# Performance work log

Measured on AMD Instinct MI355X. Metric: run time of the kernel, lower is better.

The kernel has to match this reference:

```python
import jax, jax.numpy as jnp
import numpy as np

B, L, HP, H, W = 4, 32, 32, 64, 64
D, DFFN, MAXL = 32, 64, 128

def setup_inputs() -> dict:
    key = jax.random.key(0)
    ks = jax.random.split(key, 20)
    rn = lambda k, s, sc=0.1: jax.random.normal(k, s, jnp.float32) * sc
    return {
        'x': jax.random.normal(ks[0], (B, 2 * L * HP, H, W), jnp.float32),
        'in_proj_w': rn(ks[1], (D, 12)), 'in_proj_b': rn(ks[2], (D,)),
        'layer_emb': rn(ks[3], (MAXL, D)),
        'time_decay': rn(ks[4], (D,)), 'time_first': rn(ks[5], (D,)),
        'ln_tm_g': jnp.ones((D,)), 'ln_tm_b': jnp.zeros((D,)),
        'tm_r': rn(ks[6], (D, D)), 'tm_k': rn(ks[7], (D, D)),
        'tm_v': rn(ks[8], (D, D)), 'tm_out': rn(ks[9], (D, D)),
        'ln_cm_g': jnp.ones((D,)), 'ln_cm_b': jnp.zeros((D,)),
        'cm_k': rn(ks[10], (DFFN, D)), 'cm_v': rn(ks[11], (D, DFFN)), 'cm_r': rn(ks[12], (D, D)),
        'gate_w': rn(ks[13], (1, D)), 'gate_b': rn(ks[14], (1,)),
        'row_w': rn(ks[15], (H, D)), 'row_b': rn(ks[16], (H,)),
        'col_w': rn(ks[17], (W, D)), 'col_b': rn(ks[18], (W,)),
    }

def _ln(x, g, b, eps=1e-5):
    mu = x.mean(-1, keepdims=True)
    var = ((x - mu) ** 2).mean(-1, keepdims=True)
    return (x - mu) * jax.lax.rsqrt(var + eps) * g + b

def _stats(a, b):
    # a, b: [B, L, HP, H, W] -> [B, L, HP, 12]
    af = a.reshape(*a.shape[:-2], -1)
    bf = b.reshape(*b.shape[:-2], -1)
    hs = lambda f: jnp.stack([f.mean(-1), f.std(-1, ddof=1), f.min(-1), f.max(-1)], -1)
    d = af - bf
    dm = d.mean(-1, keepdims=True)
    ds = d.std(-1, ddof=1, keepdims=True)
    dl2 = jnp.linalg.norm(d, axis=-1, keepdims=True)
    na = jnp.maximum(jnp.linalg.norm(af, axis=-1), 1e-8)
    nb = jnp.maximum(jnp.linalg.norm(bf, axis=-1), 1e-8)
    cos = ((af * bf).sum(-1) / (na * nb))[..., None]
    return jnp.concatenate([hs(af), hs(bf), dm, ds, dl2, cos], -1)

def reference(x, in_proj_w, in_proj_b, layer_emb, time_decay, time_first,
              ln_tm_g, ln_tm_b, tm_r, tm_k, tm_v, tm_out,
              ln_cm_g, ln_cm_b, cm_k, cm_v, cm_r,
              gate_w, gate_b, row_w, row_b, col_w, col_b):
    n = L * HP
    a = x[:, :n].reshape(B, L, HP, H, W)
    b = x[:, n:].reshape(B, L, HP, H, W)
    stats = _stats(a, b)                                   # [B,L,HP,12]
    feat_in = jnp.einsum('blhs,ds->blhd', stats, in_proj_w) + in_proj_b \
        + layer_emb[:L][None, :, None, :]
    feat_in = jnp.transpose(feat_in, (1, 0, 2, 3))         # [L,B,HP,D]
    wdec = jnp.exp(time_decay)

    def step(state, f):
        aa, bb, pp = state
        xn = _ln(f, ln_tm_g, ln_tm_b)
        r = jax.nn.sigmoid(xn @ tm_r.T)
        k = xn @ tm_k.T
        v = xn @ tm_v.T
        ww = time_first + k
        p = jnp.maximum(pp, ww)
        e1 = jnp.exp(pp - p)
        e2 = jnp.exp(ww - p)
        wkv = (e1 * aa + e2 * v) / jnp.maximum(e1 * bb + e2, 1e-8)
        ww2 = pp - wdec
        p2 = jnp.maximum(ww2, k)
        e1b = jnp.exp(ww2 - p2)
        e2b = jnp.exp(k - p2)
        y = f + r * (wkv @ tm_out.T)
        xn2 = _ln(y, ln_cm_g, ln_cm_b)
        kk = jnp.square(jax.nn.relu(xn2 @ cm_k.T))
        y = y + jax.nn.sigmoid(xn2 @ cm_r.T) * (kk @ cm_v.T)
        return (e1b * aa + e2b * v, e1b * bb + e2b, p2), y

    z = jnp.zeros((B, HP, D), x.dtype)
    init = (z, z, jnp.full((B, HP, D), -1e30, x.dtype))
    _, feats = jax.lax.scan(step, init, feat_in)           # [L,B,HP,D]

    gate = feats @ gate_w.T + gate_b                       # [L,B,HP,1]
    row = feats @ row_w.T + row_b                          # [L,B,HP,H]
    col = feats @ col_w.T + col_b                          # [L,B,HP,W]
    mask = jax.nn.sigmoid(gate[..., None] + row[..., None] + col[..., None, :])
    aT = jnp.transpose(a, (1, 0, 2, 3, 4))
    bT = jnp.transpose(b, (1, 0, 2, 3, 4))
    merged = mask * aT + (1.0 - mask) * bT                 # [L,B,HP,H,W]
    mixed = jnp.transpose(merged, (1, 0, 2, 3, 4)).reshape(B, n, H, W)
    return mixed, jax.nn.sigmoid(gate).mean(), mask.mean()
```

## Files before the change

### kernel.cpp

```cpp
#include <hip/hip_runtime.h>
#include <math.h>


__device__ __forceinline__ float sigf(float v) { return 1.0f / (1.0f + __expf(-v)); }

__device__ __forceinline__ float bl(float v, int l) {
    return __int_as_float(__builtin_amdgcn_readlane(__float_as_int(v), l));
}

__global__ __launch_bounds__(256) void k_stats(
    const float* __restrict__ x, const float* __restrict__ in_proj_w,
    const float* __restrict__ in_proj_b, const float* __restrict__ layer_emb,
    float* __restrict__ feat)
{
    __shared__ float red[4][9];
    __shared__ float tot[9];
    const int bid = blockIdx.x;
    const int hp = bid & 31, l = (bid >> 5) & 31, bb = bid >> 10;
    const float4* pa = (const float4*)(x + (size_t)(bb * 2048 + l * 32 + hp) * 4096);
    const float4* pb = (const float4*)(x + (size_t)(bb * 2048 + 1024 + l * 32 + hp) * 4096);
    const int t = threadIdx.x;

    float sa = 0.f, saa = 0.f, sb = 0.f, sbb = 0.f, sab = 0.f;
    float mna = 3.4e38f, mxa = -3.4e38f, mnb = 3.4e38f, mxb = -3.4e38f;
#pragma unroll
    for (int it = 0; it < 4; ++it) {
        float4 a4 = pa[t + it * 256];
        float4 b4 = pb[t + it * 256];
        sa  += a4.x + a4.y + a4.z + a4.w;
        sb  += b4.x + b4.y + b4.z + b4.w;
        saa += a4.x * a4.x + a4.y * a4.y + a4.z * a4.z + a4.w * a4.w;
        sbb += b4.x * b4.x + b4.y * b4.y + b4.z * b4.z + b4.w * b4.w;
        sab += a4.x * b4.x + a4.y * b4.y + a4.z * b4.z + a4.w * b4.w;
        mna = fminf(mna, fminf(fminf(a4.x, a4.y), fminf(a4.z, a4.w)));
        mxa = fmaxf(mxa, fmaxf(fmaxf(a4.x, a4.y), fmaxf(a4.z, a4.w)));
        mnb = fminf(mnb, fminf(fminf(b4.x, b4.y), fminf(b4.z, b4.w)));
        mxb = fmaxf(mxb, fmaxf(fmaxf(b4.x, b4.y), fmaxf(b4.z, b4.w)));
    }
#pragma unroll
    for (int m = 1; m < 64; m <<= 1) {
        sa  += __shfl_xor(sa, m);
        saa += __shfl_xor(saa, m);
        sb  += __shfl_xor(sb, m);
        sbb += __shfl_xor(sbb, m);
        sab += __shfl_xor(sab, m);
        mna = fminf(mna, __shfl_xor(mna, m));
        mxa = fmaxf(mxa, __shfl_xor(mxa, m));
        mnb = fminf(mnb, __shfl_xor(mnb, m));
        mxb = fmaxf(mxb, __shfl_xor(mxb, m));
    }
    const int lane = t & 63, wv = t >> 6;
    if (lane == 0) {
        red[wv][0] = sa;  red[wv][1] = saa; red[wv][2] = sb;  red[wv][3] = sbb;
        red[wv][4] = sab; red[wv][5] = mna; red[wv][6] = mxa; red[wv][7] = mnb;
        red[wv][8] = mxb;
    }
    __syncthreads();
    if (t == 0) {
#pragma unroll
        for (int q = 0; q < 5; ++q) tot[q] = red[0][q] + red[1][q] + red[2][q] + red[3][q];
        tot[5] = fminf(fminf(red[0][5], red[1][5]), fminf(red[2][5], red[3][5]));
        tot[6] = fmaxf(fmaxf(red[0][6], red[1][6]), fmaxf(red[2][6], red[3][6]));
        tot[7] = fminf(fminf(red[0][7], red[1][7]), fminf(red[2][7], red[3][7]));
        tot[8] = fmaxf(fmaxf(red[0][8], red[1][8]), fmaxf(red[2][8], red[3][8]));
    }
    __syncthreads();
    if (t < 32) {
        const float SA = tot[0], SAA = tot[1], SB = tot[2], SBB = tot[3], SAB = tot[4];
        const float inv_n = 1.f / 4096.f, inv_nm1 = 1.f / 4095.f;
        float st[12];
        st[0] = SA * inv_n;
        st[1] = sqrtf(fmaxf(SAA - SA * SA * inv_n, 0.f) * inv_nm1);
        st[2] = tot[5]; st[3] = tot[6];
        st[4] = SB * inv_n;
        st[5] = sqrtf(fmaxf(SBB - SB * SB * inv_n, 0.f) * inv_nm1);
        st[6] = tot[7]; st[7] = tot[8];
        const float SD = SA - SB, SDD = SAA - 2.f * SAB + SBB;
        st[8]  = SD * inv_n;
        st[9]  = sqrtf(fmaxf(SDD - SD * SD * inv_n, 0.f) * inv_nm1);
        st[10] = sqrtf(fmaxf(SDD, 0.f));
        const float na = fmaxf(sqrtf(SAA), 1e-8f), nb2 = fmaxf(sqrtf(SBB), 1e-8f);
        st[11] = SAB / (na * nb2);
        float acc = in_proj_b[t] + layer_emb[l * 32 + t];
#pragma unroll
        for (int s2 = 0; s2 < 12; ++s2) acc += st[s2] * in_proj_w[t * 12 + s2];
        feat[((l * 4 + bb) * 32 + hp) * 32 + t] = acc;
    }
}

__global__ __launch_bounds__(64, 1) void k_scan(
    const float* __restrict__ feat,
    const float* __restrict__ time_decay, const float* __restrict__ time_first,
    const float* __restrict__ ln_tm_g, const float* __restrict__ ln_tm_b,
    const float* __restrict__ tm_r, const float* __restrict__ tm_k,
    const float* __restrict__ tm_v, const float* __restrict__ tm_out,
    const float* __restrict__ ln_cm_g, const float* __restrict__ ln_cm_b,
    const float* __restrict__ cm_k, const float* __restrict__ cm_v,
    const float* __restrict__ cm_r, float* __restrict__ feats_out)
{
    const int t = threadIdx.x;
    const int d = t & 31;

    float w_r[32], w_k[32], w_v[32], w_o[32], w_cr[32], w_ck[32], w_cv[64];
    {
        const float4* pr = (const float4*)(tm_r  + d * 32);
        const float4* pk = (const float4*)(tm_k  + d * 32);
        const float4* pv = (const float4*)(tm_v  + d * 32);
        const float4* po = (const float4*)(tm_out + d * 32);
        const float4* pc = (const float4*)(cm_r  + d * 32);
        const float4* pq = (const float4*)(cm_k  + t * 32);
        const float4* pw = (const float4*)(cm_v  + d * 64);
#pragma unroll
        for (int jq = 0; jq < 8; ++jq) {
            float4 v;
            v = pr[jq]; w_r[4*jq] = v.x; w_r[4*jq+1] = v.y; w_r[4*jq+2] = v.z; w_r[4*jq+3] = v.w;
            v = pk[jq]; w_k[4*jq] = v.x; w_k[4*jq+1] = v.y; w_k[4*jq+2] = v.z; w_k[4*jq+3] = v.w;
            v = pv[jq]; w_v[4*jq] = v.x; w_v[4*jq+1] = v.y; w_v[4*jq+2] = v.z; w_v[4*jq+3] = v.w;
            v = po[jq]; w_o[4*jq] = v.x; w_o[4*jq+1] = v.y; w_o[4*jq+2] = v.z; w_o[4*jq+3] = v.w;
            v = pc[jq]; w_cr[4*jq] = v.x; w_cr[4*jq+1] = v.y; w_cr[4*jq+2] = v.z; w_cr[4*jq+3] = v.w;
            v = pq[jq]; w_ck[4*jq] = v.x; w_ck[4*jq+1] = v.y; w_ck[4*jq+2] = v.z; w_ck[4*jq+3] = v.w;
        }
#pragma unroll
        for (int jq = 0; jq < 16; ++jq) {
            float4 v = pw[jq];
            w_cv[4*jq] = v.x; w_cv[4*jq+1] = v.y; w_cv[4*jq+2] = v.z; w_cv[4*jq+3] = v.w;
        }
    }
    const float gt = ln_tm_g[d], bt = ln_tm_b[d];
    const float gc = ln_cm_g[d], bc = ln_cm_b[d];
    const float tf = time_first[d];
    const float wd = __expf(time_decay[d]);
    const int seq = blockIdx.x;
    const int bb = seq >> 5, hp = seq & 31;
    const int base = (bb * 32 + hp) * 32 + d;

    float aa = 0.f, bbs = 0.f, pp = -1e30f;
    float f = feat[base];

    for (int l = 0; l < 32; ++l) {
        float fnext = 0.f;
        if (l < 31) fnext = feat[base + (l + 1) * 4096];
        float s = f, q = f * f;
#pragma unroll
        for (int m = 1; m < 32; m <<= 1) { s += __shfl_xor(s, m, 32); q += __shfl_xor(q, m, 32); }
        const float mu = s * (1.f / 32.f);
        const float var = fmaxf(q * (1.f / 32.f) - mu * mu, 0.f);
        const float xn = (f - mu) * rsqrtf(var + 1e-5f) * gt + bt;
        float racc = 0.f, kacc = 0.f, vacc = 0.f;
#pragma unroll
        for (int j = 0; j < 32; ++j) {
            const float xj = bl(xn, j);
            racc += xj * w_r[j];
            kacc += xj * w_k[j];
            vacc += xj * w_v[j];
        }
        const float r = sigf(racc);
        const float k = kacc, v = vacc;
        const float ww = tf + k;
        const float p = fmaxf(pp, ww);
        const float e1 = __expf(pp - p), e2 = __expf(ww - p);
        const float wkv = (e1 * aa + e2 * v) / fmaxf(e1 * bbs + e2, 1e-8f);
        const float ww2 = pp - wd;
        const float p2 = fmaxf(ww2, k);
        const float e1b = __expf(ww2 - p2), e2b = __expf(k - p2);
        aa = e1b * aa + e2b * v;
        bbs = e1b * bbs + e2b;
        pp = p2;
        float oacc = 0.f;
#pragma unroll
        for (int j = 0; j < 32; ++j) oacc += bl(wkv, j) * w_o[j];
        const float y = f + r * oacc;
        float s2 = y, q2 = y * y;
#pragma unroll
        for (int m = 1; m < 32; m <<= 1) { s2 += __shfl_xor(s2, m, 32); q2 += __shfl_xor(q2, m, 32); }
        const float mu2 = s2 * (1.f / 32.f);
        const float var2 = fmaxf(q2 * (1.f / 32.f) - mu2 * mu2, 0.f);
        const float xn2 = (y - mu2) * rsqrtf(var2 + 1e-5f) * gc + bc;
        float ck = 0.f, cracc = 0.f;
#pragma unroll
        for (int j = 0; j < 32; ++j) {
            const float xj = bl(xn2, j);
            ck    += xj * w_ck[j];
            cracc += xj * w_cr[j];
        }
        float kkv = fmaxf(ck, 0.f);
        kkv *= kkv;
        float cv0 = 0.f, cv1 = 0.f;
#pragma unroll
        for (int e = 0; e < 64; e += 2) {
            cv0 += bl(kkv, e)     * w_cv[e];
            cv1 += bl(kkv, e + 1) * w_cv[e + 1];
        }
        const float y2 = y + sigf(cracc) * (cv0 + cv1);
        if (t < 32) feats_out[base + l * 4096] = y2;
        f = fnext;
    }
}

__global__ __launch_bounds__(256) void k_merge(
    const float* __restrict__ x, const float* __restrict__ feats,
    const float* __restrict__ gate_w, const float* __restrict__ gate_b,
    const float* __restrict__ row_w, const float* __restrict__ row_b,
    const float* __restrict__ col_w, const float* __restrict__ col_b,
    float* __restrict__ out, float* __restrict__ gpart, float* __restrict__ mpart)
{
    __shared__ float fs[32];
    __shared__ float row_s[64], col_s[64];
    __shared__ float gate_sh;
    __shared__ float red[4];
    const int bid = blockIdx.x;
    const int hp = bid & 31, l = (bid >> 5) & 31, bb = bid >> 10;
    const int t = threadIdx.x;

    if (t < 32) fs[t] = feats[((l * 4 + bb) * 32 + hp) * 32 + t];
    __syncthreads();
    if (t < 64) {
        float acc = row_b[t];
#pragma unroll
        for (int d2 = 0; d2 < 32; ++d2) acc += fs[d2] * row_w[t * 32 + d2];
        row_s[t] = acc;
    } else if (t < 128) {
        const int w = t - 64;
        float acc = col_b[w];
#pragma unroll
        for (int d2 = 0; d2 < 32; ++d2) acc += fs[d2] * col_w[w * 32 + d2];
        col_s[w] = acc;
    } else if (t == 128) {
        float acc = gate_b[0];
#pragma unroll
        for (int d2 = 0; d2 < 32; ++d2) acc += fs[d2] * gate_w[d2];
        gate_sh = acc;
    }
    __syncthreads();
    const float gate = gate_sh;
    const float4* pa = (const float4*)(x + (size_t)(bb * 2048 + l * 32 + hp) * 4096);
    const float4* pb = (const float4*)(x + (size_t)(bb * 2048 + 1024 + l * 32 + hp) * 4096);
    float4* po = (float4*)(out + (size_t)(bb * 1024 + l * 32 + hp) * 4096);

    float msum = 0.f;
#pragma unroll
    for (int it = 0; it < 4; ++it) {
        const int i = t + it * 256;
        const float4 a4 = pa[i];
        const float4 b4 = pb[i];
        const int h = i >> 4, w0 = (i & 15) * 4;
        const float gr = gate + row_s[h];
        const float m0 = sigf(gr + col_s[w0 + 0]);
        const float m1 = sigf(gr + col_s[w0 + 1]);
        const float m2 = sigf(gr + col_s[w0 + 2]);
        const float m3 = sigf(gr + col_s[w0 + 3]);
        float4 o;
        o.x = b4.x + m0 * (a4.x - b4.x);
        o.y = b4.y + m1 * (a4.y - b4.y);
        o.z = b4.z + m2 * (a4.z - b4.z);
        o.w = b4.w + m3 * (a4.w - b4.w);
        po[i] = o;
        msum += m0 + m1 + m2 + m3;
    }
#pragma unroll
    for (int m = 1; m < 64; m <<= 1) msum += __shfl_xor(msum, m);
    if ((t & 63) == 0) red[t >> 6] = msum;
    __syncthreads();
    if (t == 0) {
        mpart[bid] = red[0] + red[1] + red[2] + red[3];
        gpart[bid] = sigf(gate);
    }
}

__global__ __launch_bounds__(256) void k_final(
    const float* __restrict__ gpart, const float* __restrict__ mpart,
    float* __restrict__ out)
{
    __shared__ float rg[4], rm[4];
    const int t = threadIdx.x;
    float gs = 0.f, ms = 0.f;
    for (int i = t; i < 4096; i += 256) { gs += gpart[i]; ms += mpart[i]; }
#pragma unroll
    for (int m = 1; m < 64; m <<= 1) { gs += __shfl_xor(gs, m); ms += __shfl_xor(ms, m); }
    if ((t & 63) == 0) { rg[t >> 6] = gs; rm[t >> 6] = ms; }
    __syncthreads();
    if (t == 0) {
        out[16777216] = (rg[0] + rg[1] + rg[2] + rg[3]) * (1.f / 4096.f);
        out[16777217] = (rm[0] + rm[1] + rm[2] + rm[3]) * (1.f / 16777216.f);
    }
}

extern "C" void kernel_launch(void* const* d_in, const int* in_sizes, int n_in,
                              void* d_out, int out_size, void* d_ws, size_t ws_size,
                              hipStream_t stream) {
    const float* x          = (const float*)d_in[0];
    const float* in_proj_w  = (const float*)d_in[1];
    const float* in_proj_b  = (const float*)d_in[2];
    const float* layer_emb  = (const float*)d_in[3];
    const float* time_decay = (const float*)d_in[4];
    const float* time_first = (const float*)d_in[5];
    const float* ln_tm_g    = (const float*)d_in[6];
    const float* ln_tm_b    = (const float*)d_in[7];
    const float* tm_r       = (const float*)d_in[8];
    const float* tm_k       = (const float*)d_in[9];
    const float* tm_v       = (const float*)d_in[10];
    const float* tm_out     = (const float*)d_in[11];
    const float* ln_cm_g    = (const float*)d_in[12];
    const float* ln_cm_b    = (const float*)d_in[13];
    const float* cm_k       = (const float*)d_in[14];
    const float* cm_v       = (const float*)d_in[15];
    const float* cm_r       = (const float*)d_in[16];
    const float* gate_w     = (const float*)d_in[17];
    const float* gate_b     = (const float*)d_in[18];
    const float* row_w      = (const float*)d_in[19];
    const float* row_b      = (const float*)d_in[20];
    const float* col_w      = (const float*)d_in[21];
    const float* col_b      = (const float*)d_in[22];
    float* out = (float*)d_out;

    float* wsf   = (float*)d_ws;
    float* feat  = wsf;
    float* fy    = wsf + 131072;
    float* gpart = wsf + 262144;
    float* mpart = wsf + 266240;

    k_stats<<<dim3(4096), dim3(256), 0, stream>>>(x, in_proj_w, in_proj_b, layer_emb, feat);
    k_scan<<<dim3(128), dim3(64), 0, stream>>>(feat, time_decay, time_first,
                                               ln_tm_g, ln_tm_b, tm_r, tm_k, tm_v, tm_out,
                                               ln_cm_g, ln_cm_b, cm_k, cm_v, cm_r, fy);
    k_merge<<<dim3(4096), dim3(256), 0, stream>>>(x, fy, gate_w, gate_b,
                                                  row_w, row_b, col_w, col_b,
                                                  out, gpart, mpart);
    k_final<<<dim3(1), dim3(256), 0, stream>>>(gpart, mpart, out);
}
```

Baseline: 336.5 us.

## Hoist per-layer projections out of sequential scan into parallel stat and merge kernels

The per-layer work does not depend on the previous layer's output, so only the WKV state recurrence is truly sequential. The LayerNorm and r/k/v projections move into the stats kernel. The output projection, channel-mix FFN and second LayerNorm move into the merge kernel. A small elementwise kernel, one thread per channel, runs the WKV recurrence. This removes the latency-bound 128-block serial scan full of cross-lane matvecs, at the cost of extra workspace traffic for f/r/k/v/wkv and more barriers in the merge kernel.

```diff
diff --git a/kernel.cpp b/kernel.cpp
--- a/kernel.cpp
+++ b/kernel.cpp
@@ -3,23 +3,25 @@
 
 
 __device__ __forceinline__ float sigf(float v) { return 1.0f / (1.0f + __expf(-v)); }
-
-__device__ __forceinline__ float bl(float v, int l) {
-    return __int_as_float(__builtin_amdgcn_readlane(__float_as_int(v), l));
-}
 
 __global__ __launch_bounds__(256) void k_stats(
     const float* __restrict__ x, const float* __restrict__ in_proj_w,
     const float* __restrict__ in_proj_b, const float* __restrict__ layer_emb,
-    float* __restrict__ feat)
+    const float* __restrict__ ln_tm_g, const float* __restrict__ ln_tm_b,
+    const float* __restrict__ tm_r, const float* __restrict__ tm_k,
+    const float* __restrict__ tm_v,
+    float* __restrict__ f_out, float* __restrict__ r_out,
+    float* __restrict__ k_out, float* __restrict__ v_out)
 {
     __shared__ float red[4][9];
     __shared__ float tot[9];
+    __shared__ __align__(16) float xn_s[32];
     const int bid = blockIdx.x;
     const int hp = bid & 31, l = (bid >> 5) & 31, bb = bid >> 10;
     const float4* pa = (const float4*)(x + (size_t)(bb * 2048 + l * 32 + hp) * 4096);
     const float4* pb = (const float4*)(x + (size_t)(bb * 2048 + 1024 + l * 32 + hp) * 4096);
     const int t = threadIdx.x;
+    const int gidx = ((l * 4 + bb) * 32 + hp) * 32;
 
     float sa = 0.f, saa = 0.f, sb = 0.f, sbb = 0.f, sab = 0.f;
     float mna = 3.4e38f, mxa = -3.4e38f, mnb = 3.4e38f, mxb = -3.4e38f;
@@ -81,150 +83,186 @@
         st[10] = sqrtf(fmaxf(SDD, 0.f));
         const float na = fmaxf(sqrtf(SAA), 1e-8f), nb2 = fmaxf(sqrtf(SBB), 1e-8f);
         st[11] = SAB / (na * nb2);
-        float acc = in_proj_b[t] + layer_emb[l * 32 + t];
-#pragma unroll
-        for (int s2 = 0; s2 < 12; ++s2) acc += st[s2] * in_proj_w[t * 12 + s2];
-        feat[((l * 4 + bb) * 32 + hp) * 32 + t] = acc;
-    }
-}
-
-__global__ __launch_bounds__(64, 1) void k_scan(
-    const float* __restrict__ feat,
-    const float* __restrict__ time_decay, const float* __restrict__ time_first,
-    const float* __restrict__ ln_tm_g, const float* __restrict__ ln_tm_b,
-    const float* __restrict__ tm_r, const float* __restrict__ tm_k,
-    const float* __restrict__ tm_v, const float* __restrict__ tm_out,
-    const float* __restrict__ ln_cm_g, const float* __restrict__ ln_cm_b,
-    const float* __restrict__ cm_k, const float* __restrict__ cm_v,
-    const float* __restrict__ cm_r, float* __restrict__ feats_out)
-{
-    const int t = threadIdx.x;
-    const int d = t & 31;
-
-    float w_r[32], w_k[32], w_v[32], w_o[32], w_cr[32], w_ck[32], w_cv[64];
-    {
-        const float4* pr = (const float4*)(tm_r  + d * 32);
-        const float4* pk = (const float4*)(tm_k  + d * 32);
-        const float4* pv = (const float4*)(tm_v  + d * 32);
-        const float4* po = (const float4*)(tm_out + d * 32);
-        const float4* pc = (const float4*)(cm_r  + d * 32);
-        const float4* pq = (const float4*)(cm_k  + t * 32);
-        const float4* pw = (const float4*)(cm_v  + d * 64);
-#pragma unroll
-        for (int jq = 0; jq < 8; ++jq) {
-            float4 v;
-            v = pr[jq]; w_r[4*jq] = v.x; w_r[4*jq+1] = v.y; w_r[4*jq+2] = v.z; w_r[4*jq+3] = v.w;
-            v = pk[jq]; w_k[4*jq] = v.x; w_k[4*jq+1] = v.y; w_k[4*jq+2] = v.z; w_k[4*jq+3] = v.w;
-            v = pv[jq]; w_v[4*jq] = v.x; w_v[4*jq+1] = v.y; w_v[4*jq+2] = v.z; w_v[4*jq+3] = v.w;
-            v = po[jq]; w_o[4*jq] = v.x; w_o[4*jq+1] = v.y; w_o[4*jq+2] = v.z; w_o[4*jq+3] = v.w;
-            v = pc[jq]; w_cr[4*jq] = v.x; w_cr[4*jq+1] = v.y; w_cr[4*jq+2] = v.z; w_cr[4*jq+3] = v.w;
-            v = pq[jq]; w_ck[4*jq] = v.x; w_ck[4*jq+1] = v.y; w_ck[4*jq+2] = v.z; w_ck[4*jq+3] = v.w;
-        }
-#pragma unroll
-        for (int jq = 0; jq < 16; ++jq) {
-            float4 v = pw[jq];
-            w_cv[4*jq] = v.x; w_cv[4*jq+1] = v.y; w_cv[4*jq+2] = v.z; w_cv[4*jq+3] = v.w;
-        }
-    }
-    const float gt = ln_tm_g[d], bt = ln_tm_b[d];
-    const float gc = ln_cm_g[d], bc = ln_cm_b[d];
-    const float tf = time_first[d];
-    const float wd = __expf(time_decay[d]);
-    const int seq = blockIdx.x;
-    const int bb = seq >> 5, hp = seq & 31;
-    const int base = (bb * 32 + hp) * 32 + d;
-
-    float aa = 0.f, bbs = 0.f, pp = -1e30f;
-    float f = feat[base];
-
-    for (int l = 0; l < 32; ++l) {
-        float fnext = 0.f;
-        if (l < 31) fnext = feat[base + (l + 1) * 4096];
-        float s = f, q = f * f;
+        float fv = in_proj_b[t] + layer_emb[l * 32 + t];
+#pragma unroll
+        for (int s2 = 0; s2 < 12; ++s2) fv += st[s2] * in_proj_w[t * 12 + s2];
+        f_out[gidx + t] = fv;
+        float s = fv, q = fv * fv;
 #pragma unroll
         for (int m = 1; m < 32; m <<= 1) { s += __shfl_xor(s, m, 32); q += __shfl_xor(q, m, 32); }
         const float mu = s * (1.f / 32.f);
         const float var = fmaxf(q * (1.f / 32.f) - mu * mu, 0.f);
-        const float xn = (f - mu) * rsqrtf(var + 1e-5f) * gt + bt;
-        float racc = 0.f, kacc = 0.f, vacc = 0.f;
-#pragma unroll
-        for (int j = 0; j < 32; ++j) {
-            const float xj = bl(xn, j);
-            racc += xj * w_r[j];
-            kacc += xj * w_k[j];
-            vacc += xj * w_v[j];
-        }
-        const float r = sigf(racc);
-        const float k = kacc, v = vacc;
-        const float ww = tf + k;
+        xn_s[t] = (fv - mu) * rsqrtf(var + 1e-5f) * ln_tm_g[t] + ln_tm_b[t];
+    }
+    __syncthreads();
+    if (t < 96) {
+        const int d = t & 31;
+        const float* wrow = (t < 32 ? tm_r : (t < 64 ? tm_k : tm_v)) + d * 32;
+        const float4* w4 = (const float4*)wrow;
+        const float4* x4 = (const float4*)xn_s;
+        float a0 = 0.f, a1 = 0.f, a2 = 0.f, a3 = 0.f;
+#pragma unroll
+        for (int jq = 0; jq < 2; ++jq) {
+            float4 w, xv;
+            w = w4[jq];     xv = x4[jq];     a0 += w.x*xv.x + w.y*xv.y + w.z*xv.z + w.w*xv.w;
+            w = w4[jq + 2]; xv = x4[jq + 2]; a1 += w.x*xv.x + w.y*xv.y + w.z*xv.z + w.w*xv.w;
+            w = w4[jq + 4]; xv = x4[jq + 4]; a2 += w.x*xv.x + w.y*xv.y + w.z*xv.z + w.w*xv.w;
+            w = w4[jq + 6]; xv = x4[jq + 6]; a3 += w.x*xv.x + w.y*xv.y + w.z*xv.z + w.w*xv.w;
+        }
+        const float dot = (a0 + a1) + (a2 + a3);
+        if (t < 32)      r_out[gidx + d] = sigf(dot);
+        else if (t < 64) k_out[gidx + d] = dot;
+        else             v_out[gidx + d] = dot;
+    }
+}
+
+__global__ __launch_bounds__(256) void k_wkv(
+    const float* __restrict__ k_in, const float* __restrict__ v_in,
+    const float* __restrict__ time_decay, const float* __restrict__ time_first,
+    float* __restrict__ wkv_out)
+{
+    const int ch = blockIdx.x * 256 + threadIdx.x;
+    const int d = ch & 31;
+    const float tf = time_first[d];
+    const float wd = __expf(time_decay[d]);
+    float aa = 0.f, bbs = 0.f, pp = -1e30f;
+    float kc = k_in[ch], vc = v_in[ch];
+#pragma unroll 4
+    for (int l = 0; l < 32; ++l) {
+        float kn = 0.f, vn = 0.f;
+        if (l < 31) { kn = k_in[(l + 1) * 4096 + ch]; vn = v_in[(l + 1) * 4096 + ch]; }
+        const float ww = tf + kc;
         const float p = fmaxf(pp, ww);
         const float e1 = __expf(pp - p), e2 = __expf(ww - p);
-        const float wkv = (e1 * aa + e2 * v) / fmaxf(e1 * bbs + e2, 1e-8f);
+        wkv_out[l * 4096 + ch] = (e1 * aa + e2 * vc) / fmaxf(e1 * bbs + e2, 1e-8f);
         const float ww2 = pp - wd;
-        const float p2 = fmaxf(ww2, k);
-        const float e1b = __expf(ww2 - p2), e2b = __expf(k - p2);
-        aa = e1b * aa + e2b * v;
+        const float p2 = fmaxf(ww2, kc);
+        const float e1b = __expf(ww2 - p2), e2b = __expf(kc - p2);
+        aa = e1b * aa + e2b * vc;
         bbs = e1b * bbs + e2b;
         pp = p2;
-        float oacc = 0.f;
-#pragma unroll
-        for (int j = 0; j < 32; ++j) oacc += bl(wkv, j) * w_o[j];
-        const float y = f + r * oacc;
-        float s2 = y, q2 = y * y;
-#pragma unroll
-        for (int m = 1; m < 32; m <<= 1) { s2 += __shfl_xor(s2, m, 32); q2 += __shfl_xor(q2, m, 32); }
-        const float mu2 = s2 * (1.f / 32.f);
-        const float var2 = fmaxf(q2 * (1.f / 32.f) - mu2 * mu2, 0.f);
-        const float xn2 = (y - mu2) * rsqrtf(var2 + 1e-5f) * gc + bc;
-        float ck = 0.f, cracc = 0.f;
-#pragma unroll
-        for (int j = 0; j < 32; ++j) {
-            const float xj = bl(xn2, j);
-            ck    += xj * w_ck[j];
-            cracc += xj * w_cr[j];
-        }
-        float kkv = fmaxf(ck, 0.f);
-        kkv *= kkv;
-        float cv0 = 0.f, cv1 = 0.f;
-#pragma unroll
-        for (int e = 0; e < 64; e += 2) {
-            cv0 += bl(kkv, e)     * w_cv[e];
-            cv1 += bl(kkv, e + 1) * w_cv[e + 1];
-        }
-        const float y2 = y + sigf(cracc) * (cv0 + cv1);
-        if (t < 32) feats_out[base + l * 4096] = y2;
-        f = fnext;
+        kc = kn; vc = vn;
     }
 }
 
 __global__ __launch_bounds__(256) void k_merge(
-    const float* __restrict__ x, const float* __restrict__ feats,
+    const float* __restrict__ x,
+    const float* __restrict__ f_in, const float* __restrict__ r_in,
+    const float* __restrict__ wkv_in,
+    const float* __restrict__ tm_out,
+    const float* __restrict__ ln_cm_g, const float* __restrict__ ln_cm_b,
+    const float* __restrict__ cm_k, const float* __restrict__ cm_v,
+    const float* __restrict__ cm_r,
     const float* __restrict__ gate_w, const float* __restrict__ gate_b,
     const float* __restrict__ row_w, const float* __restrict__ row_b,
     const float* __restrict__ col_w, const float* __restrict__ col_b,
     float* __restrict__ out, float* __restrict__ gpart, float* __restrict__ mpart)
 {
+    __shared__ __align__(16) float wkv_s[32];
+    __shared__ __align__(16) float xn2_s[32];
+    __shared__ __align__(16) float kk_s[64];
+    __shared__ float cr_s[32];
     __shared__ float fs[32];
     __shared__ float row_s[64], col_s[64];
     __shared__ float gate_sh;
-    __shared__ float red[4];
+    __shared__ float red2[4];
     const int bid = blockIdx.x;
     const int hp = bid & 31, l = (bid >> 5) & 31, bb = bid >> 10;
     const int t = threadIdx.x;
-
-    if (t < 32) fs[t] = feats[((l * 4 + bb) * 32 + hp) * 32 + t];
+    const int gidx = ((l * 4 + bb) * 32 + hp) * 32;
+
+    if (t < 32) wkv_s[t] = wkv_in[gidx + t];
+    __syncthreads();
+    float yv = 0.f;
+    if (t < 32) {
+        const float fv = f_in[gidx + t];
+        const float rv = r_in[gidx + t];
+        const float4* w4 = (const float4*)(tm_out + t * 32);
+        const float4* x4 = (const float4*)wkv_s;
+        float a0 = 0.f, a1 = 0.f, a2 = 0.f, a3 = 0.f;
+#pragma unroll
+        for (int jq = 0; jq < 2; ++jq) {
+            float4 w, xv;
+            w = w4[jq];     xv = x4[jq];     a0 += w.x*xv.x + w.y*xv.y + w.z*xv.z + w.w*xv.w;
+            w = w4[jq + 2]; xv = x4[jq + 2]; a1 += w.x*xv.x + w.y*xv.y + w.z*xv.z + w.w*xv.w;
+            w = w4[jq + 4]; xv = x4[jq + 4]; a2 += w.x*xv.x + w.y*xv.y + w.z*xv.z + w.w*xv.w;
+            w = w4[jq + 6]; xv = x4[jq + 6]; a3 += w.x*xv.x + w.y*xv.y + w.z*xv.z + w.w*xv.w;
+        }
+        yv = fv + rv * ((a0 + a1) + (a2 + a3));
+        float s = yv, q = yv * yv;
+#pragma unroll
+        for (int m = 1; m < 32; m <<= 1) { s += __shfl_xor(s, m, 32); q += __shfl_xor(q, m, 32); }
+        const float mu = s * (1.f / 32.f);
+        const float var = fmaxf(q * (1.f / 32.f) - mu * mu, 0.f);
+        xn2_s[t] = (yv - mu) * rsqrtf(var + 1e-5f) * ln_cm_g[t] + ln_cm_b[t];
+    }
     __syncthreads();
     if (t < 64) {
-        float acc = row_b[t];
-#pragma unroll
-        for (int d2 = 0; d2 < 32; ++d2) acc += fs[d2] * row_w[t * 32 + d2];
-        row_s[t] = acc;
+        const float4* w4 = (const float4*)(cm_k + t * 32);
+        const float4* x4 = (const float4*)xn2_s;
+        float a0 = 0.f, a1 = 0.f, a2 = 0.f, a3 = 0.f;
+#pragma unroll
+        for (int jq = 0; jq < 2; ++jq) {
+            float4 w, xv;
+            w = w4[jq];     xv = x4[jq];     a0 += w.x*xv.x + w.y*xv.y + w.z*xv.z + w.w*xv.w;
+            w = w4[jq + 2]; xv = x4[jq + 2]; a1 += w.x*xv.x + w.y*xv.y + w.z*xv.z + w.w*xv.w;
+            w = w4[jq + 4]; xv = x4[jq + 4]; a2 += w.x*xv.x + w.y*xv.y + w.z*xv.z + w.w*xv.w;
+            w = w4[jq + 6]; xv = x4[jq + 6]; a3 += w.x*xv.x + w.y*xv.y + w.z*xv.z + w.w*xv.w;
+        }
+        float kk = fmaxf((a0 + a1) + (a2 + a3), 0.f);
+        kk_s[t] = kk * kk;
+    } else if (t < 96) {
+        const int d = t - 64;
+        const float4* w4 = (const float4*)(cm_r + d * 32);
+        const float4* x4 = (const float4*)xn2_s;
+        float a0 = 0.f, a1 = 0.f, a2 = 0.f, a3 = 0.f;
+#pragma unroll
+        for (int jq = 0; jq < 2; ++jq) {
+            float4 w, xv;
+            w = w4[jq];     xv = x4[jq];     a0 += w.x*xv.x + w.y*xv.y + w.z*xv.z + w.w*xv.w;
+            w = w4[jq + 2]; xv = x4[jq + 2]; a1 += w.x*xv.x + w.y*xv.y + w.z*xv.z + w.w*xv.w;
+            w = w4[jq + 4]; xv = x4[jq + 4]; a2 += w.x*xv.x + w.y*xv.y + w.z*xv.z + w.w*xv.w;
+            w = w4[jq + 6]; xv = x4[jq + 6]; a3 += w.x*xv.x + w.y*xv.y + w.z*xv.z + w.w*xv.w;
+        }
+        cr_s[d] = sigf((a0 + a1) + (a2 + a3));
+    }
+    __syncthreads();
+    if (t < 32) {
+        const float4* w4 = (const float4*)(cm_v + t * 64);
+        const float4* x4 = (const float4*)kk_s;
+        float a0 = 0.f, a1 = 0.f, a2 = 0.f, a3 = 0.f;
+#pragma unroll
+        for (int jq = 0; jq < 4; ++jq) {
+            float4 w, xv;
+            w = w4[jq];      xv = x4[jq];      a0 += w.x*xv.x + w.y*xv.y + w.z*xv.z + w.w*xv.w;
+            w = w4[jq + 4];  xv = x4[jq + 4];  a1 += w.x*xv.x + w.y*xv.y + w.z*xv.z + w.w*xv.w;
+            w = w4[jq + 8];  xv = x4[jq + 8];  a2 += w.x*xv.x + w.y*xv.y + w.z*xv.z + w.w*xv.w;
+            w = w4[jq + 12]; xv = x4[jq + 12]; a3 += w.x*xv.x + w.y*xv.y + w.z*xv.z + w.w*xv.w;
+        }
+        fs[t] = yv + cr_s[t] * ((a0 + a1) + (a2 + a3));
+    }
+    __syncthreads();
+    if (t < 64) {
+        float a0 = row_b[t], a1 = 0.f, a2 = 0.f, a3 = 0.f;
+#pragma unroll
+        for (int d2 = 0; d2 < 8; ++d2) {
+            a0 += fs[d2]      * row_w[t * 32 + d2];
+            a1 += fs[d2 + 8]  * row_w[t * 32 + d2 + 8];
+            a2 += fs[d2 + 16] * row_w[t * 32 + d2 + 16];
+            a3 += fs[d2 + 24] * row_w[t * 32 + d2 + 24];
+        }
+        row_s[t] = (a0 + a1) + (a2 + a3);
     } else if (t < 128) {
         const int w = t - 64;
-        float acc = col_b[w];
-#pragma unroll
-        for (int d2 = 0; d2 < 32; ++d2) acc += fs[d2] * col_w[w * 32 + d2];
-        col_s[w] = acc;
+        float a0 = col_b[w], a1 = 0.f, a2 = 0.f, a3 = 0.f;
+#pragma unroll
+        for (int d2 = 0; d2 < 8; ++d2) {
+            a0 += fs[d2]      * col_w[w * 32 + d2];
+            a1 += fs[d2 + 8]  * col_w[w * 32 + d2 + 8];
+            a2 += fs[d2 + 16] * col_w[w * 32 + d2 + 16];
+            a3 += fs[d2 + 24] * col_w[w * 32 + d2 + 24];
+        }
+        col_s[w] = (a0 + a1) + (a2 + a3);
     } else if (t == 128) {
         float acc = gate_b[0];
 #pragma unroll
@@ -259,10 +297,10 @@
     }
 #pragma unroll
     for (int m = 1; m < 64; m <<= 1) msum += __shfl_xor(msum, m);
-    if ((t & 63) == 0) red[t >> 6] = msum;
+    if ((t & 63) == 0) red2[t >> 6] = msum;
     __syncthreads();
     if (t == 0) {
-        mpart[bid] = red[0] + red[1] + red[2] + red[3];
+        mpart[bid] = red2[0] + red2[1] + red2[2] + red2[3];
         gpart[bid] = sigf(gate);
     }
 }
@@ -314,17 +352,20 @@
     float* out = (float*)d_out;
 
     float* wsf   = (float*)d_ws;
-    float* feat  = wsf;
-    float* fy    = wsf + 131072;
-    float* gpart = wsf + 262144;
-    float* mpart = wsf + 266240;
-
-    k_stats<<<dim3(4096), dim3(256), 0, stream>>>(x, in_proj_w, in_proj_b, layer_emb, feat);
-    k_scan<<<dim3(128), dim3(64), 0, stream>>>(feat, time_decay, time_first,
-                                               ln_tm_g, ln_tm_b, tm_r, tm_k, tm_v, tm_out,
-                                               ln_cm_g, ln_cm_b, cm_k, cm_v, cm_r, fy);
-    k_merge<<<dim3(4096), dim3(256), 0, stream>>>(x, fy, gate_w, gate_b,
-                                                  row_w, row_b, col_w, col_b,
-                                                  out, gpart, mpart);
+    float* f_ws   = wsf;
+    float* r_ws   = wsf + 131072;
+    float* k_ws   = wsf + 262144;
+    float* v_ws   = wsf + 393216;
+    float* wkv_ws = wsf + 524288;
+    float* gpart  = wsf + 655360;
+    float* mpart  = wsf + 659456;
+
+    k_stats<<<dim3(4096), dim3(256), 0, stream>>>(
+        x, in_proj_w, in_proj_b, layer_emb, ln_tm_g, ln_tm_b,
+        tm_r, tm_k, tm_v, f_ws, r_ws, k_ws, v_ws);
+    k_wkv<<<dim3(16), dim3(256), 0, stream>>>(k_ws, v_ws, time_decay, time_first, wkv_ws);
+    k_merge<<<dim3(4096), dim3(256), 0, stream>>>(
+        x, f_ws, r_ws, wkv_ws, tm_out, ln_cm_g, ln_cm_b, cm_k, cm_v, cm_r,
+        gate_w, gate_b, row_w, row_b, col_w, col_b, out, gpart, mpart);
     k_final<<<dim3(1), dim3(256), 0, stream>>>(gpart, mpart, out);
 }
```

Measured after the change: 296.2 us. 1.14x faster.
